# Performance work log

Measured on AMD Instinct MI355X. Metric: run time of the kernel, lower is better.

## Reference

```python
import jax, jax.numpy as jnp
import numpy as np
from jax import lax

K = 3          # kernel_size
G = 8          # group count in SIFA
EPS = 1e-5     # BN and GN eps


def _bn(x, g, b, m, v):
    # eval-mode BatchNorm2d over channel dim 1
    scale = (g / jnp.sqrt(v + EPS))[None, :, None, None]
    shift = (b - m * g / jnp.sqrt(v + EPS))[None, :, None, None]
    return x * scale + shift


def setup_inputs() -> dict:
    key = jax.random.key(0)
    ks = jax.random.split(key, 20)
    B, C, H, W, OUP = 8, 64, 128, 128, 128
    CE = C * K * K  # expanded channels = 576
    CG = C // G     # channels per group view = 8
    f32 = jnp.float32
    inp = {
        "x": jax.random.normal(ks[0], (B, C, H, W), f32),
        # depthwise generate conv: groups=C, out=C*K^2 -> OIHW [CE,1,K,K]
        "gen_w": jax.random.normal(ks[1], (CE, 1, K, K), f32) * 0.1,
        "gen_bn_g": jnp.ones((CE,), f32) + 0.1 * jax.random.normal(ks[2], (CE,), f32),
        "gen_bn_b": 0.1 * jax.random.normal(ks[3], (CE,), f32),
        "gen_bn_m": 0.05 * jax.random.normal(ks[4], (CE,), f32),
        "gen_bn_v": jax.random.uniform(ks[5], (CE,), f32, 0.5, 1.5),
        # GroupNorm(num_groups=CG, num_channels=CG) affine params
        "gn_w": jnp.ones((CG,), f32) + 0.1 * jax.random.normal(ks[6], (CG,), f32),
        "gn_b": 0.1 * jax.random.normal(ks[7], (CG,), f32),
        # gating params, shape (1, CG, 1, 1)
        "cweight": 0.1 * jax.random.normal(ks[8], (1, CG, 1, 1), f32),
        "cbias": jnp.ones((1, CG, 1, 1), f32) + 0.1 * jax.random.normal(ks[9], (1, CG, 1, 1), f32),
        "sweight": 0.1 * jax.random.normal(ks[10], (1, CG, 1, 1), f32),
        "sbias": jnp.ones((1, CG, 1, 1), f32) + 0.1 * jax.random.normal(ks[11], (1, CG, 1, 1), f32),
        "weights_add": jnp.asarray(0.5, f32),
        # final Conv: C -> OUP, k=K, s=K, p=0, bias=False + BN + SiLU
        "conv_w": jax.random.normal(ks[12], (OUP, C, K, K), f32) * (1.0 / np.sqrt(C * K * K)),
        "conv_bn_g": jnp.ones((OUP,), f32) + 0.1 * jax.random.normal(ks[13], (OUP,), f32),
        "conv_bn_b": 0.1 * jax.random.normal(ks[14], (OUP,), f32),
        "conv_bn_m": 0.05 * jax.random.normal(ks[15], (OUP,), f32),
        "conv_bn_v": jax.random.uniform(ks[16], (OUP,), f32, 0.5, 1.5),
    }
    return inp


def reference(x, gen_w, gen_bn_g, gen_bn_b, gen_bn_m, gen_bn_v,
              gn_w, gn_b, cweight, cbias, sweight, sbias, weights_add,
              conv_w, conv_bn_g, conv_bn_b, conv_bn_m, conv_bn_v):
    B, C, H, W = x.shape
    # --- generate: depthwise conv (groups=C) + BN + ReLU ---
    y = lax.conv_general_dilated(
        x, gen_w, window_strides=(1, 1), padding=[(K // 2, K // 2)] * 2,
        feature_group_count=C,
        dimension_numbers=("NCHW", "OIHW", "NCHW"))  # [B, C*K*K, H, W]
    y = jax.nn.relu(_bn(y, gen_bn_g, gen_bn_b, gen_bn_m, gen_bn_v))
    # --- rearrange 'b c (n1 n2) h w -> b c (h n1) (w n2)' ---
    y = y.reshape(B, C, K, K, H, W)          # (b, c, n1, n2, h, w)
    y = y.transpose(0, 1, 4, 2, 5, 3)        # (b, c, h, n1, w, n2)
    HK, WK = H * K, W * K
    y = y.reshape(B, C, HK, WK)
    # --- group view: (b*G, C//G, HK, WK) ---
    g = y.reshape(B * G, C // G, HK, WK)
    # channel gate: global avg pool -> affine -> sigmoid
    x_ch = jnp.mean(g, axis=(2, 3), keepdims=True)        # [B*G, CG, 1, 1]
    ch = g * jax.nn.sigmoid(cweight * x_ch + cbias)
    # spatial gate: per-channel GroupNorm (num_groups == num_channels)
    mu = jnp.mean(g, axis=(2, 3), keepdims=True)
    var = jnp.var(g, axis=(2, 3), keepdims=True)
    gnorm = (g - mu) / jnp.sqrt(var + EPS)
    gnorm = gnorm * gn_w[None, :, None, None] + gn_b[None, :, None, None]
    sp = g * jax.nn.sigmoid(sweight * gnorm + sbias)
    out = weights_add * ch + (1.0 - weights_add) * sp
    out = out.reshape(B, C, HK, WK)
    # --- final Conv: k=K, s=K, p=0, no bias + BN + SiLU ---
    z = lax.conv_general_dilated(
        out, conv_w, window_strides=(K, K), padding="VALID",
        dimension_numbers=("NCHW", "OIHW", "NCHW"))       # [B, OUP, H, W]
    z = _bn(z, conv_bn_g, conv_bn_b, conv_bn_m, conv_bn_v)
    return z * jax.nn.sigmoid(z)  # SiLU
```

## Files before the change

### kernel.cpp

```cpp
#include <hip/hip_runtime.h>
#include <math.h>


#define EPSF 1e-5f
typedef _Float16 v8h __attribute__((ext_vector_type(8)));
typedef __fp16 fp16x2 __attribute__((ext_vector_type(2)));
typedef float v4f __attribute__((ext_vector_type(4)));

static constexpr int C_ = 64, HW_ = 16384, W_ = 128;

static constexpr int WS_WFOLD = 0;
static constexpr int WS_SHIFT = 5184;
static constexpr int WS_BIAS  = 5760;
static constexpr int WS_GATE  = 5888;
static constexpr int WS_PART  = 7936;
static constexpr int WS_WH    = 12032;

__device__ __forceinline__ float sigmf(float v) { return 1.f / (1.f + __expf(-v)); }

__global__ __launch_bounds__(256) void k_fold(
    const float* __restrict__ gen_w,
    const float* __restrict__ gg, const float* __restrict__ gb,
    const float* __restrict__ gm, const float* __restrict__ gv,
    const float* __restrict__ conv_w,
    const float* __restrict__ cg, const float* __restrict__ cb,
    const float* __restrict__ cm, const float* __restrict__ cv,
    float* __restrict__ ws)
{
    int idx = blockIdx.x * 256 + threadIdx.x;
    _Float16* Whp = (_Float16*)(ws + WS_WH);
    if (idx < 131072) {
        int oup = idx >> 10, kk = idx & 1023, c = kk >> 4, j = kk & 15;
        float s = cg[oup] * rsqrtf(cv[oup] + EPSF);
        float v = (j < 9) ? conv_w[(oup * C_ + c) * 9 + j] * s : 0.f;
        Whp[idx] = (_Float16)v;
    } else if (idx < 136256) {
        int i = idx - 131072; int ce = i / 9;
        float s = gg[ce] * rsqrtf(gv[ce] + EPSF);
        ws[WS_WFOLD + i] = gen_w[i] * s;
    } else if (idx < 136832) {
        int ce = idx - 136256;
        float s = gg[ce] * rsqrtf(gv[ce] + EPSF);
        ws[WS_SHIFT + ce] = gb[ce] - gm[ce] * s;
    } else if (idx < 136960) {
        int oup = idx - 136832;
        float s = cg[oup] * rsqrtf(cv[oup] + EPSF);
        ws[WS_BIAS + oup] = cb[oup] - cm[oup] * s;
    }
}

__global__ __launch_bounds__(256) void k_stats(
    const float* __restrict__ x, const float* __restrict__ ws,
    float* __restrict__ part)
{
    __shared__ float xs[34 * 132];
    __shared__ __align__(16) float wfl[84];
    __shared__ float shl[9];
    __shared__ float r1[256], r2[256];
    int bid = blockIdx.x; int b = bid >> 8; int c = (bid >> 2) & 63; int q = bid & 3;
    int t = threadIdx.x;
    const float* xp = x + (size_t)(b * C_ + c) * HW_;
    for (int i = t; i < 4420; i += 256) {
        int r = i / 130, cc = i - r * 130;
        int yy = q * 32 + r - 1, xx = cc - 1;
        float v = 0.f;
        if (yy >= 0 && yy < 128 && xx >= 0 && xx < 128) v = xp[yy * 128 + xx];
        xs[r * 132 + cc] = v;
    }
    if (t < 84) wfl[t] = ws[WS_WFOLD + c * 81 + ((t < 81) ? t : 80)];
    if (t >= 84 && t < 93) shl[t - 84] = ws[WS_SHIFT + c * 9 + (t - 84)];
    __syncthreads();

    float wv[84];
#pragma unroll
    for (int i = 0; i < 21; ++i) *(float4*)&wv[i * 4] = *(const float4*)&wfl[i * 4];
    float sh9[9];
#pragma unroll
    for (int i = 0; i < 9; ++i) sh9[i] = shl[i];

    float s1 = 0.f, s2 = 0.f;
    for (int i = 0; i < 16; ++i) {
        int id = i * 256 + t; int row = id >> 7, col = id & 127;
        float nb[9];
#pragma unroll
        for (int dy = 0; dy < 3; ++dy)
#pragma unroll
            for (int dx = 0; dx < 3; ++dx) nb[dy * 3 + dx] = xs[(row + dy) * 132 + col + dx];
        float uv[9];
#pragma unroll
        for (int j = 0; j < 9; ++j) uv[j] = sh9[j];
#pragma unroll
        for (int k = 0; k < 9; ++k) {
            float xv = nb[k];
#pragma unroll
            for (int j = 0; j < 9; ++j) uv[j] = fmaf(wv[j * 9 + k], xv, uv[j]);
        }
#pragma unroll
        for (int j = 0; j < 9; ++j) {
            float v = fmaxf(uv[j], 0.f);
            s1 += v; s2 = fmaf(v, v, s2);
        }
    }
    r1[t] = s1; r2[t] = s2;
    __syncthreads();
    for (int s = 128; s > 0; s >>= 1) {
        if (t < s) { r1[t] += r1[t + s]; r2[t] += r2[t + s]; }
        __syncthreads();
    }
    if (t == 0) { part[bid * 2] = r1[0]; part[bid * 2 + 1] = r2[0]; }
}

__global__ __launch_bounds__(256) void k_gate(
    const float* __restrict__ part,
    const float* __restrict__ cwt, const float* __restrict__ cbs,
    const float* __restrict__ swt, const float* __restrict__ sbs,
    const float* __restrict__ gnw, const float* __restrict__ gnb,
    const float* __restrict__ wadd, float4* __restrict__ gate)
{
    int i = blockIdx.x * 256 + threadIdx.x;
    if (i >= 512) return;
    int b = i >> 6, c = i & 63;
    float s1 = 0.f, s2 = 0.f;
    for (int q = 0; q < 4; ++q) {
        int pi = (b * 256 + c * 4 + q) * 2;
        s1 += part[pi]; s2 += part[pi + 1];
    }
    const float N = 9.f * 16384.f;
    float mean = s1 / N;
    float var = s2 / N - mean * mean;
    float inv = rsqrtf(var + EPSF);
    int cgi = c & 7;
    float wa = wadd[0];
    float cgt = sigmf(cwt[cgi] * mean + cbs[cgi]);
    const float NL2E = -1.44269504f;
    float4 o;
    o.x = wa * cgt;
    o.y = 1.f - wa;
    o.z = NL2E * (swt[cgi] * gnw[cgi] * inv);
    o.w = NL2E * (swt[cgi] * (gnb[cgi] - mean * inv * gnw[cgi]) + sbs[cgi]);
    gate[i] = o;
}

__global__ __launch_bounds__(256) void k_main(
    const float* __restrict__ x, const float* __restrict__ ws,
    float* __restrict__ out)
{
    __shared__ _Float16 u_s[128 * 64];
    __shared__ _Float16 W_s[128 * 64];
    __shared__ float xs[2][4 * 200];
    __shared__ float bias_s[128];

    int t = threadIdx.x;
    int bid = blockIdx.x;
    int b = bid >> 7, tile = bid & 127;
    int oh0 = (tile >> 3) << 3;
    int ow0 = (tile & 7) << 4;
    if (t < 128) bias_s[t] = ws[WS_BIAS + t];

    const float* xb = x + (size_t)b * C_ * HW_;
    const _Float16* Wh = (const _Float16*)(ws + WS_WH);

    int w = __builtin_amdgcn_readfirstlane(t >> 6);
    int lane = t & 63, quad = lane >> 4, l15 = lane & 15;
    int col = lane & 15, prow0 = (lane >> 4) << 1;

    v4f acc[4][4];
#pragma unroll
    for (int a = 0; a < 4; ++a)
#pragma unroll
        for (int bb = 0; bb < 4; ++bb) acc[a][bb] = (v4f)0.f;

    {
        const float* xc = xb + (size_t)w * HW_;
#pragma unroll
        for (int i = 0; i < 3; ++i) {
            int item = lane + i * 64;
            if (item < 180) {
                int r = item / 18, cl = item - r * 18;
                int yy = oh0 + r - 1, xx = ow0 + cl - 1;
                float v = 0.f;
                if (yy >= 0 && yy < 128 && xx >= 0 && xx < 128) v = xc[yy * 128 + xx];
                xs[0][w * 200 + r * 20 + cl] = v;
            }
        }
    }
    __syncthreads();

    int buf = 0;
    for (int it = 0; it < 16; ++it) {
        int c = it * 4 + w;

        float4 wld[4];
#pragma unroll
        for (int i = 0; i < 4; ++i) {
            int id = t + i * 256; int oup = id >> 3, kb = id & 7;
            wld[i] = *(const float4*)(Wh + oup * 1024 + it * 64 + kb * 8);
        }

        const float* xw = &xs[buf][w * 200];
        float nb[12];
#pragma unroll
        for (int dr = 0; dr < 4; ++dr)
#pragma unroll
            for (int dc = 0; dc < 3; ++dc)
                nb[dr * 3 + dc] = xw[(prow0 + dr) * 20 + col + dc];

        const float* wfp = ws + WS_WFOLD + c * 81;
        const float* shp = ws + WS_SHIFT + c * 9;
        float4 g4 = *(const float4*)(ws + WS_GATE + (((b << 6) + c) << 2));

        int p0 = prow0 * 16 + col;
        int swzA0 = ((2 * w) ^ (p0 & 7)) << 3;
        int swzA1 = ((2 * w) ^ ((p0 + 16) & 7)) << 3;
        int swzB0 = ((2 * w + 1) ^ (p0 & 7)) << 3;
        int swzB1 = ((2 * w + 1) ^ ((p0 + 16) & 7)) << 3;

#pragma unroll 1
        for (int jp = 0; jp < 4; ++jp) {
            float wl[18];
#pragma unroll
            for (int i = 0; i < 18; ++i) wl[i] = wfp[jp * 18 + i];
            float s0 = shp[jp * 2], s1v = shp[jp * 2 + 1];
#pragma unroll
            for (int px = 0; px < 2; ++px) {
                float a0 = s0, a1 = s1v;
#pragma unroll
                for (int k = 0; k < 9; ++k) {
                    float xv = nb[(px + k / 3) * 3 + (k % 3)];
                    a0 = fmaf(wl[k], xv, a0);
                    a1 = fmaf(wl[9 + k], xv, a1);
                }
                float v0 = fmaxf(a0, 0.f), v1 = fmaxf(a1, 0.f);
                float e0 = __builtin_amdgcn_exp2f(fmaf(g4.z, v0, g4.w));
                float e1 = __builtin_amdgcn_exp2f(fmaf(g4.z, v1, g4.w));
                float u0 = v0 * fmaf(g4.y, __builtin_amdgcn_rcpf(1.f + e0), g4.x);
                float u1 = v1 * fmaf(g4.y, __builtin_amdgcn_rcpf(1.f + e1), g4.x);
                int base = (p0 + px * 16) * 64 + (px ? swzA1 : swzA0);
                *(fp16x2*)&u_s[base + jp * 2] = __builtin_amdgcn_cvt_pkrtz(u0, u1);
            }
        }
        {
            float w9[9];
#pragma unroll
            for (int i = 0; i < 9; ++i) w9[i] = wfp[72 + i];
            float s8 = shp[8];
#pragma unroll
            for (int px = 0; px < 2; ++px) {
                float a0 = s8;
#pragma unroll
                for (int k = 0; k < 9; ++k)
                    a0 = fmaf(w9[k], nb[(px + k / 3) * 3 + (k % 3)], a0);
                float v0 = fmaxf(a0, 0.f);
                float e0 = __builtin_amdgcn_exp2f(fmaf(g4.z, v0, g4.w));
                float u8 = v0 * fmaf(g4.y, __builtin_amdgcn_rcpf(1.f + e0), g4.x);
                union { fp16x2 p[4]; float4 f; } z;
                z.p[0] = __builtin_amdgcn_cvt_pkrtz(u8, 0.f);
                z.p[1] = __builtin_amdgcn_cvt_pkrtz(0.f, 0.f);
                z.p[2] = z.p[1]; z.p[3] = z.p[1];
                int base = (p0 + px * 16) * 64 + (px ? swzB1 : swzB0);
                *(float4*)&u_s[base] = z.f;
            }
        }

#pragma unroll
        for (int i = 0; i < 4; ++i) {
            int id = t + i * 256; int oup = id >> 3, kb = id & 7;
            *(float4*)&W_s[oup * 64 + ((kb ^ (oup & 7)) << 3)] = wld[i];
        }
        if (it < 15) {
            const float* xc = xb + (size_t)(it * 4 + 4 + w) * HW_;
#pragma unroll
            for (int i = 0; i < 3; ++i) {
                int item = lane + i * 64;
                if (item < 180) {
                    int r = item / 18, cl = item - r * 18;
                    int yy = oh0 + r - 1, xx = ow0 + cl - 1;
                    float v = 0.f;
                    if (yy >= 0 && yy < 128 && xx >= 0 && xx < 128) v = xc[yy * 128 + xx];
                    xs[buf ^ 1][w * 200 + r * 20 + cl] = v;
                }
            }
        }
        __syncthreads();

#pragma unroll
        for (int ks = 0; ks < 2; ++ks) {
            int kb = ks * 4 + quad;
            v8h A[4], Bf[4];
#pragma unroll
            for (int a = 0; a < 4; ++a) {
                int row = ((w & 1) << 6) + (a << 4) + l15;
                A[a] = *(const v8h*)&W_s[row * 64 + ((kb ^ (row & 7)) << 3)];
            }
#pragma unroll
            for (int bb = 0; bb < 4; ++bb) {
                int row = ((w >> 1) << 6) + (bb << 4) + l15;
                Bf[bb] = *(const v8h*)&u_s[row * 64 + ((kb ^ (row & 7)) << 3)];
            }
#pragma unroll
            for (int a = 0; a < 4; ++a)
#pragma unroll
                for (int bb = 0; bb < 4; ++bb)
                    acc[a][bb] = __builtin_amdgcn_mfma_f32_16x16x32_f16(A[a], Bf[bb], acc[a][bb], 0, 0, 0);
        }
        __syncthreads();
        buf ^= 1;
    }

    size_t ob = (size_t)b * 128 * HW_;
#pragma unroll
    for (int a = 0; a < 4; ++a) {
#pragma unroll
        for (int r = 0; r < 4; ++r) {
            int oup = ((w & 1) << 6) + (a << 4) + (quad << 2) + r;
            float bo = bias_s[oup];
#pragma unroll
            for (int bb = 0; bb < 4; ++bb) {
                int p2 = ((w >> 1) << 6) + (bb << 4) + l15;
                int py2 = p2 >> 4, px2 = p2 & 15;
                float z = acc[a][bb][r] + bo;
                out[ob + (size_t)oup * HW_ + (oh0 + py2) * W_ + ow0 + px2] = z * sigmf(z);
            }
        }
    }
}

extern "C" void kernel_launch(void* const* d_in, const int* in_sizes, int n_in,
                              void* d_out, int out_size, void* d_ws, size_t ws_size,
                              hipStream_t stream)
{
    const float* x      = (const float*)d_in[0];
    const float* gen_w  = (const float*)d_in[1];
    const float* gg     = (const float*)d_in[2];
    const float* gb     = (const float*)d_in[3];
    const float* gm     = (const float*)d_in[4];
    const float* gv     = (const float*)d_in[5];
    const float* gnw    = (const float*)d_in[6];
    const float* gnb    = (const float*)d_in[7];
    const float* cwt    = (const float*)d_in[8];
    const float* cbs    = (const float*)d_in[9];
    const float* swt    = (const float*)d_in[10];
    const float* sbs    = (const float*)d_in[11];
    const float* wadd   = (const float*)d_in[12];
    const float* conv_w = (const float*)d_in[13];
    const float* cg2    = (const float*)d_in[14];
    const float* cb2    = (const float*)d_in[15];
    const float* cm2    = (const float*)d_in[16];
    const float* cv2    = (const float*)d_in[17];
    float* ws  = (float*)d_ws;
    float* out = (float*)d_out;

    k_fold<<<535, 256, 0, stream>>>(gen_w, gg, gb, gm, gv, conv_w, cg2, cb2, cm2, cv2, ws);
    k_stats<<<2048, 256, 0, stream>>>(x, ws, ws + WS_PART);
    k_gate<<<2, 256, 0, stream>>>(ws + WS_PART, cwt, cbs, swt, sbs, gnw, gnb, wadd,
                                  (float4*)(ws + WS_GATE));
    k_main<<<1024, 256, 0, stream>>>(x, ws, out);
}
```

Before: 253.6 us.

## Double-buffer u tile, load weights directly from global in MFMA layout, shuffle-reduce stats

Result: faster. 245.8 us (-3.1%).

```diff
diff --git a/kernel.cpp b/kernel.cpp
--- a/kernel.cpp
+++ b/kernel.cpp
@@ -30,7 +30,8 @@
     int idx = blockIdx.x * 256 + threadIdx.x;
     _Float16* Whp = (_Float16*)(ws + WS_WH);
     if (idx < 131072) {
-        int oup = idx >> 10, kk = idx & 1023, c = kk >> 4, j = kk & 15;
+        int kb = idx >> 10, oup = (idx >> 3) & 127, e = idx & 7;
+        int k = kb * 8 + e, c = k >> 4, j = k & 15;
         float s = cg[oup] * rsqrtf(cv[oup] + EPSF);
         float v = (j < 9) ? conv_w[(oup * C_ + c) * 9 + j] * s : 0.f;
         Whp[idx] = (_Float16)v;
@@ -56,7 +57,7 @@
     __shared__ float xs[34 * 132];
     __shared__ __align__(16) float wfl[84];
     __shared__ float shl[9];
-    __shared__ float r1[256], r2[256];
+    __shared__ float r1[4], r2[4];
     int bid = blockIdx.x; int b = bid >> 8; int c = (bid >> 2) & 63; int q = bid & 3;
     int t = threadIdx.x;
     const float* xp = x + (size_t)(b * C_ + c) * HW_;
@@ -101,13 +102,18 @@
             s1 += v; s2 = fmaf(v, v, s2);
         }
     }
-    r1[t] = s1; r2[t] = s2;
+#pragma unroll
+    for (int off = 32; off > 0; off >>= 1) {
+        s1 += __shfl_down(s1, off, 64);
+        s2 += __shfl_down(s2, off, 64);
+    }
+    int wid = t >> 6;
+    if ((t & 63) == 0) { r1[wid] = s1; r2[wid] = s2; }
     __syncthreads();
-    for (int s = 128; s > 0; s >>= 1) {
-        if (t < s) { r1[t] += r1[t + s]; r2[t] += r2[t + s]; }
-        __syncthreads();
-    }
-    if (t == 0) { part[bid * 2] = r1[0]; part[bid * 2 + 1] = r2[0]; }
+    if (t == 0) {
+        part[bid * 2]     = r1[0] + r1[1] + r1[2] + r1[3];
+        part[bid * 2 + 1] = r2[0] + r2[1] + r2[2] + r2[3];
+    }
 }
 
 __global__ __launch_bounds__(256) void k_gate(
@@ -145,8 +151,7 @@
     const float* __restrict__ x, const float* __restrict__ ws,
     float* __restrict__ out)
 {
-    __shared__ _Float16 u_s[128 * 64];
-    __shared__ _Float16 W_s[128 * 64];
+    __shared__ _Float16 u_s[2][128 * 64];
     __shared__ float xs[2][4 * 200];
     __shared__ float bias_s[128];
 
@@ -170,8 +175,8 @@
 #pragma unroll
         for (int bb = 0; bb < 4; ++bb) acc[a][bb] = (v4f)0.f;
 
-    {
-        const float* xc = xb + (size_t)w * HW_;
+    auto stage = [&](int buf, int c) {
+        const float* xc = xb + (size_t)c * HW_;
 #pragma unroll
         for (int i = 0; i < 3; ++i) {
             int item = lane + i * 64;
@@ -180,23 +185,14 @@
                 int yy = oh0 + r - 1, xx = ow0 + cl - 1;
                 float v = 0.f;
                 if (yy >= 0 && yy < 128 && xx >= 0 && xx < 128) v = xc[yy * 128 + xx];
-                xs[0][w * 200 + r * 20 + cl] = v;
-            }
-        }
-    }
-    __syncthreads();
-
-    int buf = 0;
-    for (int it = 0; it < 16; ++it) {
+                xs[buf][w * 200 + r * 20 + cl] = v;
+            }
+        }
+    };
+
+    auto uphase = [&](int it) {
+        int buf = it & 1;
         int c = it * 4 + w;
-
-        float4 wld[4];
-#pragma unroll
-        for (int i = 0; i < 4; ++i) {
-            int id = t + i * 256; int oup = id >> 3, kb = id & 7;
-            wld[i] = *(const float4*)(Wh + oup * 1024 + it * 64 + kb * 8);
-        }
-
         const float* xw = &xs[buf][w * 200];
         float nb[12];
 #pragma unroll
@@ -214,6 +210,7 @@
         int swzA1 = ((2 * w) ^ ((p0 + 16) & 7)) << 3;
         int swzB0 = ((2 * w + 1) ^ (p0 & 7)) << 3;
         int swzB1 = ((2 * w + 1) ^ ((p0 + 16) & 7)) << 3;
+        _Float16* us = u_s[buf];
 
 #pragma unroll 1
         for (int jp = 0; jp < 4; ++jp) {
@@ -236,7 +233,7 @@
                 float u0 = v0 * fmaf(g4.y, __builtin_amdgcn_rcpf(1.f + e0), g4.x);
                 float u1 = v1 * fmaf(g4.y, __builtin_amdgcn_rcpf(1.f + e1), g4.x);
                 int base = (p0 + px * 16) * 64 + (px ? swzA1 : swzA0);
-                *(fp16x2*)&u_s[base + jp * 2] = __builtin_amdgcn_cvt_pkrtz(u0, u1);
+                *(fp16x2*)&us[base + jp * 2] = __builtin_amdgcn_cvt_pkrtz(u0, u1);
             }
         }
         {
@@ -258,53 +255,48 @@
                 z.p[1] = __builtin_amdgcn_cvt_pkrtz(0.f, 0.f);
                 z.p[2] = z.p[1]; z.p[3] = z.p[1];
                 int base = (p0 + px * 16) * 64 + (px ? swzB1 : swzB0);
-                *(float4*)&u_s[base] = z.f;
-            }
-        }
-
-#pragma unroll
-        for (int i = 0; i < 4; ++i) {
-            int id = t + i * 256; int oup = id >> 3, kb = id & 7;
-            *(float4*)&W_s[oup * 64 + ((kb ^ (oup & 7)) << 3)] = wld[i];
-        }
-        if (it < 15) {
-            const float* xc = xb + (size_t)(it * 4 + 4 + w) * HW_;
-#pragma unroll
-            for (int i = 0; i < 3; ++i) {
-                int item = lane + i * 64;
-                if (item < 180) {
-                    int r = item / 18, cl = item - r * 18;
-                    int yy = oh0 + r - 1, xx = ow0 + cl - 1;
-                    float v = 0.f;
-                    if (yy >= 0 && yy < 128 && xx >= 0 && xx < 128) v = xc[yy * 128 + xx];
-                    xs[buf ^ 1][w * 200 + r * 20 + cl] = v;
-                }
-            }
-        }
-        __syncthreads();
-
+                *(float4*)&us[base] = z.f;
+            }
+        }
+    };
+
+    stage(0, w);
+    __syncthreads();
+    uphase(0);
+    stage(1, 4 + w);
+    __syncthreads();
+
+    for (int it = 0; it < 16; ++it) {
+        v8h A[2][4];
+#pragma unroll
+        for (int ks = 0; ks < 2; ++ks)
+#pragma unroll
+            for (int a = 0; a < 4; ++a) {
+                int row = ((w & 1) << 6) + (a << 4) + l15;
+                int kb = it * 8 + ks * 4 + quad;
+                A[ks][a] = *(const v8h*)(Wh + ((size_t)kb * 128 + row) * 8);
+            }
+
+        if (it < 15) uphase(it + 1);
+        if (it < 14) stage(it & 1, (it + 2) * 4 + w);
+
+        const _Float16* ub = u_s[it & 1];
 #pragma unroll
         for (int ks = 0; ks < 2; ++ks) {
             int kb = ks * 4 + quad;
-            v8h A[4], Bf[4];
-#pragma unroll
-            for (int a = 0; a < 4; ++a) {
-                int row = ((w & 1) << 6) + (a << 4) + l15;
-                A[a] = *(const v8h*)&W_s[row * 64 + ((kb ^ (row & 7)) << 3)];
-            }
+            v8h Bf[4];
 #pragma unroll
             for (int bb = 0; bb < 4; ++bb) {
                 int row = ((w >> 1) << 6) + (bb << 4) + l15;
-                Bf[bb] = *(const v8h*)&u_s[row * 64 + ((kb ^ (row & 7)) << 3)];
+                Bf[bb] = *(const v8h*)&ub[row * 64 + ((kb ^ (row & 7)) << 3)];
             }
 #pragma unroll
             for (int a = 0; a < 4; ++a)
 #pragma unroll
                 for (int bb = 0; bb < 4; ++bb)
-                    acc[a][bb] = __builtin_amdgcn_mfma_f32_16x16x32_f16(A[a], Bf[bb], acc[a][bb], 0, 0, 0);
-        }
-        __syncthreads();
-        buf ^= 1;
+                    acc[a][bb] = __builtin_amdgcn_mfma_f32_16x16x32_f16(A[ks][a], Bf[bb], acc[a][bb], 0, 0, 0);
+        }
+        if (it < 15) __syncthreads();
     }
 
     size_t ob = (size_t)b * 128 * HW_;
```
